# Optimization experiments

Measured on AMD Instinct MI355X. Metric: run time of the kernel, lower is better.

The kernel has to match this reference:

```python
import jax, jax.numpy as jnp
import numpy as np

C = 64
TOPK = 5


def conv2d(x, w, b, pad):
    y = jax.lax.conv_general_dilated(
        x, w, window_strides=(1, 1), padding=[(pad, pad), (pad, pad)],
        dimension_numbers=('NCHW', 'OIHW', 'NCHW'))
    return y + b[None, :, None, None]


def unfold3x3_reflect(x):
    # torch: F.unfold(ReflectionPad2d(1)(x), kernel_size=3) -> [B, C*9, H*W]
    B, Cc, H, W = x.shape
    xp = jnp.pad(x, ((0, 0), (0, 0), (1, 1), (1, 1)), mode='reflect')
    patches = jnp.stack(
        [xp[:, :, kh:kh + H, kw:kw + W] for kh in range(3) for kw in range(3)],
        axis=2)  # [B, C, 9, H, W], kernel order kh*3+kw matches torch unfold
    return patches.reshape(B, Cc * 9, H * W)


def fold3x3(cols, H, W):
    # torch: F.fold(cols, (H, W), kernel_size=3, padding=1) -> overlap-add
    B, D, L = cols.shape
    Cc = D // 9
    patches = cols.reshape(B, Cc, 3, 3, H, W)
    out = jnp.zeros((B, Cc, H + 2, W + 2), cols.dtype)
    for kh in range(3):
        for kw in range(3):
            out = out.at[:, :, kh:kh + H, kw:kw + W].add(patches[:, :, kh, kw])
    return out[:, :, 1:H + 1, 1:W + 1]


def setup_inputs() -> dict:
    key = jax.random.key(0)
    ks = jax.random.split(key, 9)
    B, H, W = 4, 64, 64
    x = jax.random.normal(ks[0], (B, C, H, W), jnp.float32)
    s = 0.05
    w1 = jax.random.normal(ks[1], (C, C, 3, 3), jnp.float32) * s
    b1 = jax.random.normal(ks[2], (C,), jnp.float32) * s
    w2 = jax.random.normal(ks[3], (C, C, 3, 3), jnp.float32) * s
    b2 = jax.random.normal(ks[4], (C,), jnp.float32) * s
    wt1 = jax.random.normal(ks[5], (C, C * (TOPK - 1), 1, 1), jnp.float32) * s
    bt1 = jax.random.normal(ks[6], (C,), jnp.float32) * s
    wt2 = jax.random.normal(ks[7], (C, C * 3, 1, 1), jnp.float32) * s
    bt2 = jax.random.normal(ks[8], (C,), jnp.float32) * s
    return {'x': x, 'w1': w1, 'b1': b1, 'w2': w2, 'b2': b2,
            'wt1': wt1, 'bt1': bt1, 'wt2': wt2, 'bt2': bt2}


def reference(x, w1, b1, w2, b2, wt1, bt1, wt2, bt2):
    B, Cc, H, W = x.shape
    L = H * W
    EPS = 1e-12

    feature = conv2d(jax.nn.relu(conv2d(x, w1, b1, 1)), w2, b2, 1)

    x_unfold = unfold3x3_reflect(x)                   # [B, 9C, L]
    qn = x_unfold / jnp.maximum(
        jnp.linalg.norm(x_unfold, axis=1, keepdims=True), EPS)
    kn = qn  # q and k are both x, normalized along the feature (9C) axis

    # R_qk[b, m, l] = <k patch m, q patch l>  (torch bmm(k[B,L,D], q[B,D,L]))
    R = jnp.einsum('bdm,bdl->bml', kn, qn)            # [B, L, L]
    vals, idxs = jax.lax.top_k(R.transpose(0, 2, 1), TOPK)  # over key axis
    R_maxs = vals.transpose(0, 2, 1)                  # [B, k, L]
    R_indexs = idxs.transpose(0, 2, 1)                # [B, k, L]

    Ts = []
    for i in range(1, TOPK):
        idx = R_indexs[:, i, :]                       # [B, L]
        T_unfold = jnp.take_along_axis(x_unfold, idx[:, None, :], axis=2)
        T = fold3x3(T_unfold, H, W) / 9.0             # [B, C, H, W]
        S = R_maxs[:, i, :].reshape(B, 1, H, W)
        Ts.append(T * S)

    texture = conv2d(jnp.concatenate(Ts, axis=1), wt1, bt1, 0)
    y = conv2d(jnp.concatenate([feature, x, texture], axis=1), wt2, bt2, 0)
    return y
```

## Files before the change

kernel.cpp:

```cpp
#include <hip/hip_runtime.h>
#include <hip/hip_bf16.h>
#include <hip/hip_fp8.h>
#include <stdint.h>

typedef unsigned short ushort_t;
typedef __attribute__((ext_vector_type(8))) short short8;
typedef __attribute__((ext_vector_type(16))) float f32x16;
typedef __attribute__((ext_vector_type(8))) int i32x8;
typedef __attribute__((ext_vector_type(4))) int i32x4;

#define DEV __device__ __forceinline__

DEV int refl(int j) { return j < 0 ? -j : (j > 63 ? 126 - j : j); }

DEV void gload_lds16(const void* g, void* l) {
  __builtin_amdgcn_global_load_lds(
      (const __attribute__((address_space(1))) unsigned int*)g,
      (__attribute__((address_space(3))) unsigned int*)l, 16, 0, 0);
}

DEV unsigned packval(float v, int idx) {
  unsigned u = __float_as_uint(v);
  u ^= (0x80000000u | (unsigned)((int)u >> 31));
  return (u & 0xFFFFF000u) | (unsigned)idx;
}

DEV void ins8(unsigned (&s)[8], unsigned p) {
#pragma unroll
  for (int j = 0; j < 8; ++j) {
    unsigned mx = s[j] > p ? s[j] : p;
    unsigned mn = s[j] > p ? p : s[j];
    s[j] = mx;
    p = mn;
  }
}

DEV i32x8 ldfrag(const uint8_t* p0, const uint8_t* p1) {
  i32x4 lo = *(const i32x4*)p0;
  i32x4 hi = *(const i32x4*)p1;
  i32x8 r;
  r[0] = lo[0]; r[1] = lo[1]; r[2] = lo[2]; r[3] = lo[3];
  r[4] = hi[0]; r[5] = hi[1]; r[6] = hi[2]; r[7] = hi[3];
  return r;
}

__global__ __launch_bounds__(256) void k_prep(
    const float* __restrict__ x, float* __restrict__ xt,
    const float* __restrict__ w1, const float* __restrict__ w2,
    const float* __restrict__ wt1, const float* __restrict__ bt1,
    const float* __restrict__ wt2, const float* __restrict__ bt2,
    ushort_t* __restrict__ Wb1t, ushort_t* __restrict__ Wb2t,
    float* __restrict__ Wcat, float* __restrict__ beff) {
  int t = threadIdx.x;
  if (blockIdx.x < 256) {
    __shared__ float tile[64][65];
    int wg = blockIdx.x;
    int b = wg >> 6, pt = wg & 63;
    int lane = t & 63, grp = t >> 6;
    const float* xb = x + ((size_t)b * 64) * 4096 + pt * 64;
#pragma unroll
    for (int j = 0; j < 16; ++j) {
      int c = j * 4 + grp;
      tile[c][lane] = xb[(size_t)c * 4096 + lane];
    }
    __syncthreads();
    float* xtb = xt + ((size_t)b * 4096 + (size_t)pt * 64) * 64;
#pragma unroll
    for (int j = 0; j < 16; ++j) {
      int p = j * 4 + grp;
      xtb[p * 64 + lane] = tile[lane][p];
    }
    return;
  }
  int id = (blockIdx.x - 256) * 256 + t;
  if (id < 36864) {
    int n = id & 63, d = id >> 6;
    __hip_bfloat16 h = __float2bfloat16(w1[(n * 64 + (d & 63)) * 9 + (d >> 6)]);
    Wb1t[(n >> 3) * 4608 + (d >> 5) * 256 + ((d >> 3) & 3) * 64 + (n & 7) * 8 + (d & 7)] =
        *(ushort_t*)&h;
  } else if (id < 73728) {
    int rel = id - 36864;
    int n = rel & 63, d = rel >> 6;
    __hip_bfloat16 h = __float2bfloat16(w2[(n * 64 + (d & 63)) * 9 + (d >> 6)]);
    Wb2t[(n >> 3) * 4608 + (d >> 5) * 256 + ((d >> 3) & 3) * 64 + (n & 7) * 8 + (d & 7)] =
        *(ushort_t*)&h;
  } else if (id < 81920) {
    int rel = id - 73728;
    int co = rel & 63, k = rel >> 6;
    Wcat[k * 64 + co] = wt2[co * 192 + k];
  } else if (id < 98304) {
    int rel = id - 81920;
    int co = rel & 63, j = rel >> 6;
    float s = 0.f;
    for (int ct = 0; ct < 64; ++ct) s += wt2[co * 192 + 128 + ct] * wt1[ct * 256 + j];
    Wcat[(128 + j) * 64 + co] = s;
  } else if (id < 98368) {
    int co = id - 98304;
    float s = bt2[co];
    for (int ct = 0; ct < 64; ++ct) s += wt2[co * 192 + 128 + ct] * bt1[ct];
    beff[co] = s;
  }
}

__global__ __launch_bounds__(512) void k_unfold(const float* __restrict__ xt,
                                                uint8_t* __restrict__ Xq,
                                                double* __restrict__ dinv) {
  __shared__ uint8_t U[4608];
  int rbg = blockIdx.x;
  int b = rbg >> 9, rb = rbg & 511;
  int t = threadIdx.x;
  int p = t >> 6, lane = t & 63;
  int l = rb * 8 + p;
  int y = l >> 6, xq = l & 63;
  const float* xb = xt + ((size_t)b * 4096) * 64;
  float v[9];
  double s = 0.0;
#pragma unroll
  for (int tap = 0; tap < 9; ++tap) {
    int kh = tap / 3, kw = tap % 3;
    int gy = refl(y + kh - 1), gx = refl(xq + kw - 1);
    v[tap] = xb[(gy * 64 + gx) * 64 + lane];
    s += (double)v[tap] * (double)v[tap];
  }
#pragma unroll
  for (int off = 32; off; off >>= 1) s += __shfl_xor(s, off, 64);
  double n = sqrt(s);
  if (n < 1e-12) n = 1e-12;
  if (lane == 0) dinv[b * 4096 + l] = 1.0 / n;
  float inv = (float)(1.0 / n);
#pragma unroll
  for (int tap = 0; tap < 9; ++tap) {
    __hip_fp8_e4m3 h(v[tap] * inv);
    U[tap * 512 + (lane >> 4) * 128 + p * 16 + (lane & 15)] = h.__x;
  }
  __syncthreads();
  uint8_t* g = Xq + (size_t)rbg * 4608;
  if (t < 288) *(uint4*)&g[t * 16] = *(const uint4*)&U[t * 16];
}

__global__ __launch_bounds__(256) void k_cgemm(const float* __restrict__ in_t,
                                               const ushort_t* __restrict__ Wt,
                                               const float* __restrict__ bias,
                                               float* __restrict__ out_t,
                                               int do_relu) {
  __shared__ __align__(16) ushort_t Ab[2][2048];
  __shared__ __align__(16) ushort_t Bb[2][2048];
  int t = threadIdx.x;
  int w = t >> 6, lane = t & 63, rr = lane & 31, half = lane >> 5;
  int mi = w >> 1, ni = w & 1;
  int bid = blockIdx.x;
  int b = bid >> 6, y = bid & 63;
  const float* xrow = in_t + ((size_t)b * 4096) * 64;
  int sr = t >> 2, sq = t & 3;

  float bz = bias[ni * 32 + rr];
  f32x16 acc;
#pragma unroll
  for (int q = 0; q < 16; ++q) acc[q] = bz;

#define STAGE_CONV(kc_, buf_)                                                   \
  {                                                                             \
    int tap = (kc_) >> 1, ch = ((kc_) & 1) * 32 + sq * 8;                       \
    int kh = tap / 3, kw = tap % 3;                                             \
    int gy = y + kh - 1, gx = sr + kw - 1;                                      \
    ushort_t tmp[8];                                                            \
    if (gy >= 0 && gy < 64 && gx >= 0 && gx < 64) {                             \
      const float* src = xrow + ((size_t)(gy * 64 + gx)) * 64 + ch;             \
      float4 v0 = *(const float4*)src;                                          \
      float4 v1 = *(const float4*)(src + 4);                                    \
      float vv[8] = {v0.x, v0.y, v0.z, v0.w, v1.x, v1.y, v1.z, v1.w};           \
      _Pragma("unroll") for (int j = 0; j < 8; ++j) {                           \
        __hip_bfloat16 h = __float2bfloat16(vv[j]);                             \
        tmp[j] = *(ushort_t*)&h;                                                \
      }                                                                         \
    } else {                                                                    \
      _Pragma("unroll") for (int j = 0; j < 8; ++j) tmp[j] = 0;                 \
    }                                                                           \
    *(uint4*)&Ab[buf_][(sr >> 3) * 256 + sq * 64 + (sr & 7) * 8] = *(uint4*)tmp;\
    gload_lds16(Wt + (size_t)(t >> 5) * 4608 + (kc_) * 256 + (t & 31) * 8,      \
                &Bb[buf_][t * 8]);                                              \
  }

  STAGE_CONV(0, 0)
#pragma unroll 2
  for (int kc = 0; kc < 18; ++kc) {
    __syncthreads();
    if (kc < 17) STAGE_CONV(kc + 1, (kc + 1) & 1)
    const ushort_t* tA = Ab[kc & 1];
    const ushort_t* tB = Bb[kc & 1];
#pragma unroll
    for (int ks = 0; ks < 2; ++ks) {
      int seg8 = (ks * 2 + half) * 8 + (rr & 7);
      short8 af = *(const short8*)&tA[(mi * 4 + (rr >> 3)) * 256 + seg8 * 8];
      short8 bf = *(const short8*)&tB[(ni * 4 + (rr >> 3)) * 256 + seg8 * 8];
      acc = __builtin_amdgcn_mfma_f32_32x32x16_bf16(af, bf, acc, 0, 0, 0);
    }
  }
#undef STAGE_CONV
  float* orow = out_t + ((size_t)b * 4096 + y * 64) * 64;
  int n = ni * 32 + rr;
#pragma unroll
  for (int reg = 0; reg < 16; ++reg) {
    int m = mi * 32 + (reg & 3) + 8 * (reg >> 2) + 4 * half;
    float vv = acc[reg];
    if (do_relu) vv = fmaxf(vv, 0.f);
    orow[m * 64 + n] = vv;
  }
}

__global__ __launch_bounds__(256, 4) void k_gram(const uint8_t* __restrict__ Xq,
                                                 int* __restrict__ pidx) {
  __shared__ __align__(16) char lds[40960];
  uint8_t* sAb = (uint8_t*)lds;
  uint8_t* sBb = (uint8_t*)(lds + 32768);

  int wg = blockIdx.x;
  int u = wg & 7, v = wg >> 3;
  int bs = u + 8 * (v & 1);
  int b = bs >> 2, sp = bs & 3;
  int cb = v >> 1;
  int colbase = cb * 64;
  int t = threadIdx.x;
  int w = t >> 6, lane = t & 63;
  int rr = lane & 31, half = lane >> 5;
  int rb8 = rr >> 3, r8 = rr & 7;
  int so0 = (2 * half) * 8 + r8;
  int so1 = so0 + 8;

  const uint8_t* Xb = Xq + (size_t)b * 512 * 4608;
  const uint8_t* XB = Xb + (size_t)(cb * 8) * 4608;

  unsigned list[8];
#pragma unroll
  for (int j = 0; j < 8; ++j) list[j] = 0u;

#pragma unroll 1
  for (int mt = 0; mt < 4; ++mt) {
    int rowbase = sp * 1024 + mt * 256;
    __syncthreads();
    const uint8_t* XA = Xb + (size_t)(sp * 128 + mt * 32) * 4608;
    f32x16 acc[2][2];
#pragma unroll
    for (int im = 0; im < 2; ++im)
#pragma unroll
      for (int il = 0; il < 2; ++il)
#pragma unroll
        for (int q = 0; q < 16; ++q) acc[im][il][q] = 0.f;
    {
#pragma unroll
      for (int j = 0; j < 4; ++j) {
        int s = j * 256 + t;
        gload_lds16(XA + (size_t)(s >> 5) * 4608 + (s & 31) * 16, sAb + s * 16);
      }
      gload_lds16(XB + (size_t)(t >> 5) * 4608 + (t & 31) * 16, sBb + t * 16);
    }
#pragma unroll 1
    for (int kc = 0; kc < 9; ++kc) {
      __syncthreads();
      if (kc < 8) {
        int buf = (kc + 1) & 1;
        int ko = (kc + 1) * 512;
#pragma unroll
        for (int j = 0; j < 4; ++j) {
          int s = j * 256 + t;
          gload_lds16(XA + (size_t)(s >> 5) * 4608 + ko + (s & 31) * 16,
                      sAb + buf * 16384 + s * 16);
        }
        gload_lds16(XB + (size_t)(t >> 5) * 4608 + ko + (t & 31) * 16,
                    sBb + buf * 4096 + t * 16);
      }
      const uint8_t* tA = sAb + (kc & 1) * 16384;
      const uint8_t* tB = sBb + (kc & 1) * 4096;
      i32x8 af[2], bf[2];
#pragma unroll
      for (int im = 0; im < 2; ++im) {
        int rbA = w * 8 + im * 4 + rb8;
        af[im] = ldfrag(&tA[(rbA * 32 + so0) * 16], &tA[(rbA * 32 + so1) * 16]);
      }
#pragma unroll
      for (int il = 0; il < 2; ++il) {
        int rbB = il * 4 + rb8;
        bf[il] = ldfrag(&tB[(rbB * 32 + so0) * 16], &tB[(rbB * 32 + so1) * 16]);
      }
      acc[0][0] = __builtin_amdgcn_mfma_scale_f32_32x32x64_f8f6f4(
          af[0], bf[0], acc[0][0], 0, 0, 0, 0x7F7F7F7F, 0, 0x7F7F7F7F);
      acc[0][1] = __builtin_amdgcn_mfma_scale_f32_32x32x64_f8f6f4(
          af[0], bf[1], acc[0][1], 0, 0, 0, 0x7F7F7F7F, 0, 0x7F7F7F7F);
      acc[1][0] = __builtin_amdgcn_mfma_scale_f32_32x32x64_f8f6f4(
          af[1], bf[0], acc[1][0], 0, 0, 0, 0x7F7F7F7F, 0, 0x7F7F7F7F);
      acc[1][1] = __builtin_amdgcn_mfma_scale_f32_32x32x64_f8f6f4(
          af[1], bf[1], acc[1][1], 0, 0, 0, 0x7F7F7F7F, 0, 0x7F7F7F7F);
    }
    int rowb = rowbase + w * 64;
#pragma unroll
    for (int im = 0; im < 2; ++im) {
#pragma unroll
      for (int reg = 0; reg < 16; ++reg) {
        float a0 = acc[im][0][reg], a1 = acc[im][1][reg];
        float vo = half ? a1 : a0;
        float vs = half ? a0 : a1;
        float vr = __shfl_xor(vs, 32, 64);
        int rbase = rowb + im * 32 + (reg & 3) + 8 * (reg >> 2);
        ins8(list, packval(vo, rbase + 4 * half));
        ins8(list, packval(vr, rbase + 4 * (1 - half)));
      }
    }
  }
  __syncthreads();
  unsigned* M = (unsigned*)lds;
#pragma unroll
  for (int j = 0; j < 8; ++j) M[lane * 33 + w * 8 + j] = list[j];
  __syncthreads();
  if (t < 64) {
    unsigned bl[8];
#pragma unroll
    for (int j = 0; j < 8; ++j) bl[j] = 0u;
#pragma unroll 1
    for (int i = 0; i < 32; ++i) ins8(bl, M[t * 33 + i]);
    size_t base = (((size_t)b * 4 + sp) * 4096 + colbase + t) * 8;
#pragma unroll
    for (int j = 0; j < 8; ++j) pidx[base + j] = (int)bl[j];
  }
}

__global__ __launch_bounds__(256) void k_refine(const float* __restrict__ xt,
                                                const double* __restrict__ dinv,
                                                const int* __restrict__ pidx,
                                                float* __restrict__ Sval,
                                                int* __restrict__ Sidx) {
  int w = threadIdx.x >> 6, lane = threadIdx.x & 63;
  int gl = blockIdx.x * 4 + w;
  int b = gl >> 12, l = gl & 4095;
  int y = l >> 6, xq = l & 63;
  const float* xb = xt + ((size_t)b * 4096) * 64;
  unsigned cp = 0u;
  if (lane < 32) {
    int sp = lane >> 3, j = lane & 7;
    cp = (unsigned)pidx[(((size_t)b * 4 + sp) * 4096 + l) * 8 + j];
  }
  int wm[8];
#pragma unroll
  for (int r = 0; r < 8; ++r) {
    unsigned v = cp;
#pragma unroll
    for (int off = 32; off; off >>= 1) {
      unsigned ov = __shfl_xor(v, off, 64);
      v = ov > v ? ov : v;
    }
    wm[r] = (int)(v & 4095u);
    if (cp == v) cp = 0u;
  }
  int ch4 = (lane & 15) * 4;
  float4 xl4[9];
#pragma unroll
  for (int tap = 0; tap < 9; ++tap) {
    int kh = tap / 3, kw = tap % 3;
    xl4[tap] = *(const float4*)&xb[(refl(y + kh - 1) * 64 + refl(xq + kw - 1)) * 64 + ch4];
  }
  double il = dinv[b * 4096 + l];
  double rv = -1e30;
  int ridx = 0x7fffffff;
#pragma unroll
  for (int it = 0; it < 2; ++it) {
    int m = wm[it * 4 + (lane >> 4)];
    int my = m >> 6, mx = m & 63;
    double d = 0.0;
#pragma unroll
    for (int tap = 0; tap < 9; ++tap) {
      int kh = tap / 3, kw = tap % 3;
      float4 gv = *(const float4*)&xb[(refl(my + kh - 1) * 64 + refl(mx + kw - 1)) * 64 + ch4];
      d += (double)xl4[tap].x * (double)gv.x + (double)xl4[tap].y * (double)gv.y +
           (double)xl4[tap].z * (double)gv.z + (double)xl4[tap].w * (double)gv.w;
    }
#pragma unroll
    for (int off = 1; off < 16; off <<= 1) d += __shfl_xor(d, off, 64);
    double R = d * il * dinv[b * 4096 + m];
    double Rsrc = __shfl(R, (lane & 3) * 16, 64);
    int msrc = __shfl(m, (lane & 3) * 16, 64);
    if ((lane >> 2) == it && lane < 8) { rv = Rsrc; ridx = msrc; }
  }
#pragma unroll
  for (int r = 0; r < 5; ++r) {
    double v = rv;
    int i = ridx;
#pragma unroll
    for (int off = 32; off; off >>= 1) {
      double ov = __shfl_xor(v, off, 64);
      int oi = __shfl_xor(i, off, 64);
      if (ov > v || (ov == v && oi < i)) { v = ov; i = oi; }
    }
    if (r >= 1 && lane == 0) {
      Sval[((size_t)b * 5 + r) * 4096 + l] = (float)v;
      Sidx[((size_t)b * 5 + r) * 4096 + l] = i;
    }
    if (rv == v && ridx == i) rv = -1e30;
  }
}

__global__ __launch_bounds__(256, 4) void k_out(const float* __restrict__ xt,
                                                const float* __restrict__ feat,
                                                const float* __restrict__ Sval,
                                                const int* __restrict__ Sidx,
                                                const float* __restrict__ Wcat,
                                                const float* __restrict__ beff,
                                                float* __restrict__ out) {
  __shared__ float X[16 * 388];
  __shared__ int SI[3 * 18 * 4];
  __shared__ float SV[16 * 4];
  int t = threadIdx.x;
  int w = t >> 6, lane = t & 63;
  int p0 = blockIdx.x * 16;
  int b = p0 >> 12, pl = p0 & 4095;
  int y0 = pl >> 6, x0 = pl & 63;
  if (t < 216) {
    int r = t / 72, rem = t % 72;
    int c = rem >> 2, i = (rem & 3) + 1;
    int qy = y0 - 1 + r, qx = x0 - 1 + c;
    int m = 0x7fffffff;
    if (qy >= 0 && qy < 64 && qx >= 0 && qx < 64)
      m = Sidx[((size_t)b * 5 + i) * 4096 + qy * 64 + qx] & 4095;
    SI[(r * 18 + c) * 4 + (i - 1)] = m;
  }
  if (t < 64) {
    int px = t >> 2, i = (t & 3) + 1;
    SV[px * 4 + (i - 1)] = Sval[((size_t)b * 5 + i) * 4096 + pl + px];
  }
#pragma unroll
  for (int jj = 0; jj < 4; ++jj) {
    int px = w * 4 + jj;
    X[px * 388 + lane] = feat[((size_t)b * 4096 + pl + px) * 64 + lane];
    X[px * 388 + 64 + lane] = xt[((size_t)b * 4096 + pl + px) * 64 + lane];
  }
  __syncthreads();
  const float* xb = xt + ((size_t)b * 4096) * 64;
#pragma unroll 4
  for (int k = 0; k < 16; ++k) {
    int pr = w * 16 + k;
    int px = pr >> 2, i = pr & 3;
    float a = 0.f;
#pragma unroll
    for (int tap = 0; tap < 9; ++tap) {
      int kh = tap / 3, kw = tap % 3;
      int m = SI[((2 - kh) * 18 + px + 2 - kw) * 4 + i];
      if (m != 0x7fffffff) {
        int gy = refl((m >> 6) + kh - 1), gx = refl((m & 63) + kw - 1);
        a += xb[(gy * 64 + gx) * 64 + lane];
      }
    }
    X[px * 388 + 128 + i * 64 + lane] = a * SV[px * 4 + i] * (1.f / 9.f);
  }
  __syncthreads();
  int px = t & 15, cog = t >> 4;
  float4 acc = *(const float4*)&beff[cog * 4];
#pragma unroll 2
  for (int k = 0; k < 384; k += 4) {
    float4 xv = *(const float4*)&X[px * 388 + k];
    float4 w0 = *(const float4*)&Wcat[(k + 0) * 64 + cog * 4];
    float4 w1 = *(const float4*)&Wcat[(k + 1) * 64 + cog * 4];
    float4 w2 = *(const float4*)&Wcat[(k + 2) * 64 + cog * 4];
    float4 w3 = *(const float4*)&Wcat[(k + 3) * 64 + cog * 4];
    acc.x += w0.x * xv.x + w1.x * xv.y + w2.x * xv.z + w3.x * xv.w;
    acc.y += w0.y * xv.x + w1.y * xv.y + w2.y * xv.z + w3.y * xv.w;
    acc.z += w0.z * xv.x + w1.z * xv.y + w2.z * xv.z + w3.z * xv.w;
    acc.w += w0.w * xv.x + w1.w * xv.y + w2.w * xv.z + w3.w * xv.w;
  }
  size_t ob = ((size_t)b * 64 + cog * 4) * 4096 + pl + px;
  out[ob] = acc.x;
  out[ob + 4096] = acc.y;
  out[ob + 8192] = acc.z;
  out[ob + 12288] = acc.w;
}

extern "C" void kernel_launch(void* const* d_in, const int* in_sizes, int n_in,
                              void* d_out, int out_size, void* d_ws, size_t ws_size,
                              hipStream_t stream) {
  const float* x = (const float*)d_in[0];
  const float* w1 = (const float*)d_in[1];
  const float* b1 = (const float*)d_in[2];
  const float* w2 = (const float*)d_in[3];
  const float* b2 = (const float*)d_in[4];
  const float* wt1 = (const float*)d_in[5];
  const float* bt1 = (const float*)d_in[6];
  const float* wt2 = (const float*)d_in[7];
  const float* bt2 = (const float*)d_in[8];

  char* ws = (char*)d_ws;
  float* x_t = (float*)(ws + 0);
  float* y1 = (float*)(ws + 4194304);
  float* feat = (float*)(ws + 8388608);
  uint8_t* Xq = (uint8_t*)(ws + 12582912);
  double* dinv = (double*)(ws + 31457280);
  int* pidx = (int*)(ws + 31653888);
  float* Sval = (float*)(ws + 33751040);
  int* Sidx = (int*)(ws + 34078720);
  ushort_t* Wb1t = (ushort_t*)(ws + 34406400);
  ushort_t* Wb2t = (ushort_t*)(ws + 34553856);
  float* Wcat = (float*)(ws + 34701312);
  float* beff = (float*)(ws + 34799616);
  float* out = (float*)d_out;

  k_prep<<<dim3(641), dim3(256), 0, stream>>>(x, x_t, w1, w2, wt1, bt1, wt2, bt2,
                                              Wb1t, Wb2t, Wcat, beff);
  k_unfold<<<dim3(2048), dim3(512), 0, stream>>>(x_t, Xq, dinv);
  k_cgemm<<<dim3(256), dim3(256), 0, stream>>>(x_t, Wb1t, b1, y1, 1);
  k_cgemm<<<dim3(256), dim3(256), 0, stream>>>(y1, Wb2t, b2, feat, 0);
  k_gram<<<dim3(1024), dim3(256), 0, stream>>>(Xq, pidx);
  k_refine<<<dim3(4096), dim3(256), 0, stream>>>(x_t, dinv, pidx, Sval, Sidx);
  k_out<<<dim3(1024), dim3(256), 0, stream>>>(x_t, feat, Sval, Sidx, Wcat, beff, out);
}
```

Baseline: 313.3 us.

## Split output stage into texture gather kernel and bf16 MFMA 1x1 GEMM

The fused output kernel, which gathered texture features and then ran a scalar fp32 384-wide 1x1 convolution, is split in two. k_tex writes the concatenated feature/x/texture activations as bf16 in the tiled layout the existing conv GEMM uses. k_outg does the final projection with 32x32x16 bf16 MFMA, double-buffered LDS loads and a transposed store. The folded weight Wcat becomes bf16. This trades lower FP32 ALU time for an extra launch, a global round-trip of the activations, and reduced precision in the final projection.

```diff
diff --git a/kernel.cpp b/kernel.cpp
--- a/kernel.cpp
+++ b/kernel.cpp
@@ -44,13 +44,17 @@
   return r;
 }
 
+DEV int toff(int r, int d, int rbstride) {
+  return (r >> 3) * rbstride + (d >> 5) * 256 + ((d >> 3) & 3) * 64 + (r & 7) * 8 + (d & 7);
+}
+
 __global__ __launch_bounds__(256) void k_prep(
     const float* __restrict__ x, float* __restrict__ xt,
     const float* __restrict__ w1, const float* __restrict__ w2,
     const float* __restrict__ wt1, const float* __restrict__ bt1,
     const float* __restrict__ wt2, const float* __restrict__ bt2,
     ushort_t* __restrict__ Wb1t, ushort_t* __restrict__ Wb2t,
-    float* __restrict__ Wcat, float* __restrict__ beff) {
+    ushort_t* __restrict__ Wcatb, float* __restrict__ beff) {
   int t = threadIdx.x;
   if (blockIdx.x < 256) {
     __shared__ float tile[64][65];
@@ -76,24 +80,25 @@
   if (id < 36864) {
     int n = id & 63, d = id >> 6;
     __hip_bfloat16 h = __float2bfloat16(w1[(n * 64 + (d & 63)) * 9 + (d >> 6)]);
-    Wb1t[(n >> 3) * 4608 + (d >> 5) * 256 + ((d >> 3) & 3) * 64 + (n & 7) * 8 + (d & 7)] =
-        *(ushort_t*)&h;
+    Wb1t[toff(n, d, 4608)] = *(ushort_t*)&h;
   } else if (id < 73728) {
     int rel = id - 36864;
     int n = rel & 63, d = rel >> 6;
     __hip_bfloat16 h = __float2bfloat16(w2[(n * 64 + (d & 63)) * 9 + (d >> 6)]);
-    Wb2t[(n >> 3) * 4608 + (d >> 5) * 256 + ((d >> 3) & 3) * 64 + (n & 7) * 8 + (d & 7)] =
-        *(ushort_t*)&h;
-  } else if (id < 81920) {
+    Wb2t[toff(n, d, 4608)] = *(ushort_t*)&h;
+  } else if (id < 98304) {
     int rel = id - 73728;
-    int co = rel & 63, k = rel >> 6;
-    Wcat[k * 64 + co] = wt2[co * 192 + k];
-  } else if (id < 98304) {
-    int rel = id - 81920;
-    int co = rel & 63, j = rel >> 6;
-    float s = 0.f;
-    for (int ct = 0; ct < 64; ++ct) s += wt2[co * 192 + 128 + ct] * wt1[ct * 256 + j];
-    Wcat[(128 + j) * 64 + co] = s;
+    int n = rel & 63, d = rel >> 6;
+    float s;
+    if (d < 128) {
+      s = wt2[n * 192 + d];
+    } else {
+      int j = d - 128;
+      s = 0.f;
+      for (int ct = 0; ct < 64; ++ct) s += wt2[n * 192 + 128 + ct] * wt1[ct * 256 + j];
+    }
+    __hip_bfloat16 h = __float2bfloat16(s);
+    Wcatb[toff(n, d, 3072)] = *(ushort_t*)&h;
   } else if (id < 98368) {
     int co = id - 98304;
     float s = bt2[co];
@@ -397,14 +402,12 @@
   }
 }
 
-__global__ __launch_bounds__(256, 4) void k_out(const float* __restrict__ xt,
+__global__ __launch_bounds__(256, 4) void k_tex(const float* __restrict__ xt,
                                                 const float* __restrict__ feat,
                                                 const float* __restrict__ Sval,
                                                 const int* __restrict__ Sidx,
-                                                const float* __restrict__ Wcat,
-                                                const float* __restrict__ beff,
-                                                float* __restrict__ out) {
-  __shared__ float X[16 * 388];
+                                                ushort_t* __restrict__ Xb16) {
+  __shared__ ushort_t U[6144];
   __shared__ int SI[3 * 18 * 4];
   __shared__ float SV[16 * 4];
   int t = threadIdx.x;
@@ -428,8 +431,12 @@
 #pragma unroll
   for (int jj = 0; jj < 4; ++jj) {
     int px = w * 4 + jj;
-    X[px * 388 + lane] = feat[((size_t)b * 4096 + pl + px) * 64 + lane];
-    X[px * 388 + 64 + lane] = xt[((size_t)b * 4096 + pl + px) * 64 + lane];
+    float fv = feat[((size_t)b * 4096 + pl + px) * 64 + lane];
+    float xv = xt[((size_t)b * 4096 + pl + px) * 64 + lane];
+    __hip_bfloat16 hf = __float2bfloat16(fv);
+    __hip_bfloat16 hx = __float2bfloat16(xv);
+    U[toff(px, lane, 3072)] = *(ushort_t*)&hf;
+    U[toff(px, 64 + lane, 3072)] = *(ushort_t*)&hx;
   }
   __syncthreads();
   const float* xb = xt + ((size_t)b * 4096) * 64;
@@ -447,28 +454,76 @@
         a += xb[(gy * 64 + gx) * 64 + lane];
       }
     }
-    X[px * 388 + 128 + i * 64 + lane] = a * SV[px * 4 + i] * (1.f / 9.f);
-  }
-  __syncthreads();
-  int px = t & 15, cog = t >> 4;
-  float4 acc = *(const float4*)&beff[cog * 4];
+    __hip_bfloat16 h = __float2bfloat16(a * SV[px * 4 + i] * (1.f / 9.f));
+    U[toff(px, 128 + i * 64 + lane, 3072)] = *(ushort_t*)&h;
+  }
+  __syncthreads();
+  ushort_t* g = Xb16 + (size_t)blockIdx.x * 6144;
+#pragma unroll
+  for (int i = 0; i < 3; ++i) {
+    int s = i * 256 + t;
+    *(uint4*)&g[s * 8] = *(const uint4*)&U[s * 8];
+  }
+}
+
+__global__ __launch_bounds__(256) void k_outg(const ushort_t* __restrict__ Xb16,
+                                              const ushort_t* __restrict__ Wcatb,
+                                              const float* __restrict__ beff,
+                                              float* __restrict__ out) {
+  __shared__ __align__(16) ushort_t Ab[2][2048];
+  __shared__ __align__(16) ushort_t Bb[2][2048];
+  __shared__ float T[64 * 65];
+  int t = threadIdx.x;
+  int w = t >> 6, lane = t & 63, rr = lane & 31, half = lane >> 5;
+  int mi = w >> 1, ni = w & 1;
+  int bid = blockIdx.x;
+  int b = bid >> 6, y = bid & 63;
+  const ushort_t* XA = Xb16 + (size_t)bid * 24576;
+
+  float bz = beff[ni * 32 + rr];
+  f32x16 acc;
+#pragma unroll
+  for (int q = 0; q < 16; ++q) acc[q] = bz;
+
+#define STAGE_OUT(kc_, buf_)                                                    \
+  {                                                                             \
+    gload_lds16(XA + (size_t)(t >> 5) * 3072 + (kc_) * 256 + (t & 31) * 8,      \
+                &Ab[buf_][t * 8]);                                              \
+    gload_lds16(Wcatb + (size_t)(t >> 5) * 3072 + (kc_) * 256 + (t & 31) * 8,   \
+                &Bb[buf_][t * 8]);                                              \
+  }
+
+  STAGE_OUT(0, 0)
 #pragma unroll 2
-  for (int k = 0; k < 384; k += 4) {
-    float4 xv = *(const float4*)&X[px * 388 + k];
-    float4 w0 = *(const float4*)&Wcat[(k + 0) * 64 + cog * 4];
-    float4 w1 = *(const float4*)&Wcat[(k + 1) * 64 + cog * 4];
-    float4 w2 = *(const float4*)&Wcat[(k + 2) * 64 + cog * 4];
-    float4 w3 = *(const float4*)&Wcat[(k + 3) * 64 + cog * 4];
-    acc.x += w0.x * xv.x + w1.x * xv.y + w2.x * xv.z + w3.x * xv.w;
-    acc.y += w0.y * xv.x + w1.y * xv.y + w2.y * xv.z + w3.y * xv.w;
-    acc.z += w0.z * xv.x + w1.z * xv.y + w2.z * xv.z + w3.z * xv.w;
-    acc.w += w0.w * xv.x + w1.w * xv.y + w2.w * xv.z + w3.w * xv.w;
-  }
-  size_t ob = ((size_t)b * 64 + cog * 4) * 4096 + pl + px;
-  out[ob] = acc.x;
-  out[ob + 4096] = acc.y;
-  out[ob + 8192] = acc.z;
-  out[ob + 12288] = acc.w;
+  for (int kc = 0; kc < 12; ++kc) {
+    __syncthreads();
+    if (kc < 11) STAGE_OUT(kc + 1, (kc + 1) & 1)
+    const ushort_t* tA = Ab[kc & 1];
+    const ushort_t* tB = Bb[kc & 1];
+#pragma unroll
+    for (int ks = 0; ks < 2; ++ks) {
+      int seg8 = (ks * 2 + half) * 8 + (rr & 7);
+      short8 af = *(const short8*)&tA[(mi * 4 + (rr >> 3)) * 256 + seg8 * 8];
+      short8 bf = *(const short8*)&tB[(ni * 4 + (rr >> 3)) * 256 + seg8 * 8];
+      acc = __builtin_amdgcn_mfma_f32_32x32x16_bf16(af, bf, acc, 0, 0, 0);
+    }
+  }
+#undef STAGE_OUT
+  __syncthreads();
+  int n = ni * 32 + rr;
+#pragma unroll
+  for (int reg = 0; reg < 16; ++reg) {
+    int m = mi * 32 + (reg & 3) + 8 * (reg >> 2) + 4 * half;
+    T[m * 65 + n] = acc[reg];
+  }
+  __syncthreads();
+  int n2 = t >> 2, grp = t & 3;
+  float o[16];
+#pragma unroll
+  for (int j = 0; j < 16; ++j) o[j] = T[(grp * 16 + j) * 65 + n2];
+  float* od = out + ((size_t)b * 64 + n2) * 4096 + y * 64 + grp * 16;
+#pragma unroll
+  for (int j = 0; j < 4; ++j) *(float4*)(od + j * 4) = *(float4*)&o[j * 4];
 }
 
 extern "C" void kernel_launch(void* const* d_in, const int* in_sizes, int n_in,
@@ -489,22 +544,24 @@
   float* y1 = (float*)(ws + 4194304);
   float* feat = (float*)(ws + 8388608);
   uint8_t* Xq = (uint8_t*)(ws + 12582912);
+  ushort_t* Xb16 = (ushort_t*)(ws + 12582912);
   double* dinv = (double*)(ws + 31457280);
   int* pidx = (int*)(ws + 31653888);
   float* Sval = (float*)(ws + 33751040);
   int* Sidx = (int*)(ws + 34078720);
   ushort_t* Wb1t = (ushort_t*)(ws + 34406400);
   ushort_t* Wb2t = (ushort_t*)(ws + 34553856);
-  float* Wcat = (float*)(ws + 34701312);
+  ushort_t* Wcatb = (ushort_t*)(ws + 34701312);
   float* beff = (float*)(ws + 34799616);
   float* out = (float*)d_out;
 
   k_prep<<<dim3(641), dim3(256), 0, stream>>>(x, x_t, w1, w2, wt1, bt1, wt2, bt2,
-                                              Wb1t, Wb2t, Wcat, beff);
+                                              Wb1t, Wb2t, Wcatb, beff);
   k_unfold<<<dim3(2048), dim3(512), 0, stream>>>(x_t, Xq, dinv);
   k_cgemm<<<dim3(256), dim3(256), 0, stream>>>(x_t, Wb1t, b1, y1, 1);
   k_cgemm<<<dim3(256), dim3(256), 0, stream>>>(y1, Wb2t, b2, feat, 0);
   k_gram<<<dim3(1024), dim3(256), 0, stream>>>(Xq, pidx);
   k_refine<<<dim3(4096), dim3(256), 0, stream>>>(x_t, dinv, pidx, Sval, Sidx);
-  k_out<<<dim3(1024), dim3(256), 0, stream>>>(x_t, feat, Sval, Sidx, Wcat, beff, out);
-}
+  k_tex<<<dim3(1024), dim3(256), 0, stream>>>(x_t, feat, Sval, Sidx, Xb16);
+  k_outg<<<dim3(256), dim3(256), 0, stream>>>(Xb16, Wcatb, beff, out);
+}
```

New measurement: 278.6 us. 1.12x faster.
